# Kernel tuning notes

Hardware: AMD Instinct MI355X
Metric: run time of the kernel (lower is better)

The kernel has to match this reference:

```python
import jax, jax.numpy as jnp
import numpy as np

B, T, D, K = 4, 4096, 256, 16


def hankel_eigvecs(T: int, k: int) -> jnp.ndarray:
    """Top-k |eigenvalue| eigenvectors of Z_ij = 2/((i+j)^3 - (i+j)), 1-indexed."""
    idx = np.arange(1, T + 1, dtype=np.float64)
    ij = idx[None, :] + idx[:, None]
    Z = 2.0 / (ij ** 3 - ij)
    w, v = np.linalg.eigh(Z)
    top = np.argsort(-np.abs(w))[:k]
    return jnp.asarray(v[:, top], dtype=jnp.float32)  # (T, K)


def setup_inputs() -> dict:
    key = jax.random.key(0)
    kx, kw = jax.random.split(key)
    x = jax.random.normal(kx, (B, T, D), dtype=jnp.float32)
    # Stacked weights of the K independent nn.Linear(D, D, bias=False) modules.
    # W[k] is the torch Linear weight (out, in); y = c @ W[k].T.
    W = jax.random.normal(kw, (K, D, D), dtype=jnp.float32) * (1.0 / np.sqrt(D))
    phi = hankel_eigvecs(T, K)  # Hankel eigenvector buffer (non-trainable)
    return {"x": x, "W": W, "phi": phi}


def reference(x, W, phi):
    # x: (B,T,D), W: (K,D,D), phi: (T,K)
    # c_k[t] = cumsum_{s<=t} phi[s,k] * x[s]   -> batched over all K filters
    C = jnp.cumsum(phi[None, :, :, None] * x[:, :, None, :], axis=1)  # (B,T,K,D)
    # out[t] = sum_k phi[t,k] * (c_k[t] @ W_k^T)
    out = jnp.einsum('btkd,ked,tk->bte', C, W, phi)  # (B,T,D)
    return out  # dropout is identity in eval mode (dropout=0.0)
```

## Files before the change

kernel.cpp:

```cpp
#include <hip/hip_runtime.h>


typedef __bf16 bf16x8 __attribute__((ext_vector_type(8)));
typedef float  f32x4  __attribute__((ext_vector_type(4)));
typedef unsigned short u16;
typedef unsigned int   u32;

__device__ static inline u16 f2bf(float f) {
    unsigned int u = __float_as_uint(f);
    u = (u + 0x7fffu + ((u >> 16) & 1u)) >> 16;
    return (u16)u;
}

__device__ static inline void gload16(const void* g, void* l) {
    __builtin_amdgcn_global_load_lds((const __attribute__((address_space(1))) void*)g,
                                     (__attribute__((address_space(3))) void*)l, 16, 0, 0);
}

__global__ __launch_bounds__(256) void k0_wt(const float* __restrict__ W, u16* __restrict__ WT) {
    const int e = blockIdx.x, d = threadIdx.x;
    union { u16 u[16]; uint4 v[2]; } ob;
#pragma unroll
    for (int k = 0; k < 16; ++k)
        ob.u[k] = f2bf(W[((size_t)k * 256 + e) * 256 + d]);
    uint4* dst = (uint4*)(WT + (size_t)e * 4096 + d * 16);
    dst[0] = ob.v[0]; dst[1] = ob.v[1];
}

__global__ __launch_bounds__(256) void k1_sums(const float* __restrict__ x,
                                               const float* __restrict__ phi,
                                               float* __restrict__ U) {
    __shared__ float phis[256];
    const int tid = threadIdx.x;
    const int b = blockIdx.x, c = blockIdx.y;
    const int t0 = c * 16;
    phis[tid] = phi[t0 * 16 + tid];
    __syncthreads();
    float acc[16];
#pragma unroll
    for (int k = 0; k < 16; ++k) acc[k] = 0.f;
    for (int s = 0; s < 16; ++s) {
        const float xv = x[(size_t)((b << 12) + t0 + s) * 256 + tid];
        union { float f[16]; float4 v[4]; } pv;
#pragma unroll
        for (int j = 0; j < 4; ++j) pv.v[j] = *(const float4*)&phis[s * 16 + j * 4];
#pragma unroll
        for (int k = 0; k < 16; ++k) acc[k] = fmaf(pv.f[k], xv, acc[k]);
    }
    float4* Up = (float4*)(U + ((size_t)((b * 256 + c) * 256 + tid)) * 16);
    union { float f[16]; float4 v[4]; } ov;
#pragma unroll
    for (int k = 0; k < 16; ++k) ov.f[k] = acc[k];
#pragma unroll
    for (int j = 0; j < 4; ++j) Up[j] = ov.v[j];
}

__global__ __launch_bounds__(256) void k2_scan(float* __restrict__ U) {
    const int b  = blockIdx.x;
    const int dl = threadIdx.x & 63;
    const int dk = blockIdx.y * 64 + dl;
    const int q  = threadIdx.x >> 6;
    float* base = U + (size_t)b * 1048576 + (size_t)(q * 64) * 4096 + dk;
    float s = 0.f;
#pragma unroll 8
    for (int j = 0; j < 64; ++j) s += base[(size_t)j * 4096];
    __shared__ float qs[4][64];
    qs[q][dl] = s;
    __syncthreads();
    float pre = 0.f;
#pragma unroll
    for (int i = 0; i < 4; ++i) pre += (i < q) ? qs[i][dl] : 0.f;
    float run = pre;
#pragma unroll 8
    for (int j = 0; j < 64; ++j) {
        const float v = base[(size_t)j * 4096];
        base[(size_t)j * 4096] = run;
        run += v;
    }
}

__global__ __launch_bounds__(512, 2) void k4_fused(const float* __restrict__ x,
                                                   const float* __restrict__ phi,
                                                   const float* __restrict__ U,
                                                   const u16* __restrict__ BT,
                                                   float* __restrict__ C) {
    __shared__ __align__(16) char smem[131072];
    const int tid = threadIdx.x;
    const int m0 = blockIdx.x * 128;
    const int ks = blockIdx.y;
    const int b  = m0 >> 12, t0 = m0 & 4095, c0 = t0 >> 4;
    const int w = tid >> 6, l = tid & 63;
    const int wm = (w >> 2) * 64, wn = (w & 3) * 64;
    const int lg = l >> 4, lr = l & 15;
    f32x4 acc[4][4] = {};

    const bool is_chain = (w < 4);
    const bool is_stage = (w >= 4);

    const int kp = l & 7, dl = (l >> 3) & 3, ch = (w << 1) | (l >> 5);
    const int colb = dl * 32 + kp * 4;
    float2 p01[16];
    if (is_chain) {
#pragma unroll
        for (int s = 0; s < 16; ++s)
            p01[s] = *(const float2*)&phi[(t0 + ch * 16 + s) * 16 + kp * 2];
    }

    const int tl = tid & 255;
    const char* bsrc = (const char*)BT + (size_t)(tl >> 3) * 8192 + ks * 4096
                     + (((tl & 7) * 16) ^ (((tl >> 3) & 7) << 4));
    char* const smemA = smem + 98304;

    auto stageB = [&](int kt, int bufw) {
        char* dst = smem + bufw * 32768 + tl * 16;
        const char* src = bsrc + (size_t)kt * 128;
#pragma unroll
        for (int c = 0; c < 8; ++c)
            gload16(src + (size_t)c * 262144, dst + c * 4096);
    };
    auto issueX = [&](float (&xr)[16], float2& us, int kt) {
        const int d = ks * 128 + kt * 4 + dl;
        const float* xp = x + (size_t)(m0 + ch * 16) * 256 + d;
#pragma unroll
        for (int s = 0; s < 16; ++s) xr[s] = xp[(size_t)s * 256];
        us = *(const float2*)&U[((size_t)((b * 256 + c0 + ch) * 256 + d)) * 16 + kp * 2];
    };
    auto chains = [&](const float (&xr)[16], float2 us, int abw) {
        float r0 = us.x, r1 = us.y;
        char* Ab = smemA + abw * 16384 + ch * 2048;
#pragma unroll
        for (int s = 0; s < 16; ++s) {
            r0 = fmaf(p01[s].x, xr[s], r0);
            r1 = fmaf(p01[s].y, xr[s], r1);
            const float v0 = p01[s].x * r0, v1 = p01[s].y * r1;
            u32 pk;
            asm("v_cvt_pk_bf16_f32 %0, %1, %2" : "=v"(pk) : "v"(v0), "v"(v1));
            *(u32*)(Ab + s * 128 + (colb ^ ((s & 7) << 4))) = pk;
        }
    };
    auto mfma_phase = [&](int abr, int bbr) {
        const char* Abase = smemA + abr * 16384;
        const char* Bbase = smem + bbr * 32768;
#pragma unroll
        for (int kk = 0; kk < 2; ++kk) {
            const int kb = kk * 64 + lg * 16;
            bf16x8 af[4], bfv[4];
#pragma unroll
            for (int mi = 0; mi < 4; ++mi) {
                const int r = wm + mi * 16 + lr;
                af[mi] = *(const bf16x8*)(Abase + r * 128 + (kb ^ ((r & 7) << 4)));
            }
#pragma unroll
            for (int ni = 0; ni < 4; ++ni) {
                const int n = wn + ni * 16 + lr;
                bfv[ni] = *(const bf16x8*)(Bbase + n * 128 + (kb ^ ((n & 7) << 4)));
            }
#pragma unroll
            for (int mi = 0; mi < 4; ++mi)
#pragma unroll
                for (int ni = 0; ni < 4; ++ni)
                    acc[mi][ni] = __builtin_amdgcn_mfma_f32_16x16x32_bf16(af[mi], bfv[ni], acc[mi][ni], 0, 0, 0);
        }
    };

    float xA[16], xB[16]; float2 uA, uB;
    if (is_chain) { issueX(xA, uA, 0); issueX(xB, uB, 1); }
    if (is_stage) { stageB(0, 0); stageB(1, 1); }
    __builtin_amdgcn_sched_barrier(0);
    if (is_chain) {
        chains(xA, uA, 0);
        asm volatile("s_waitcnt lgkmcnt(0)" ::: "memory");
    }
    if (is_stage) asm volatile("s_waitcnt vmcnt(8)" ::: "memory");
    asm volatile("s_barrier" ::: "memory");

    int br = 0, bw = 2;
    auto body = [&](int kt, float (&xW)[16], float2& uW,
                    const float (&xR)[16], float2 uR) {
        const int abr = kt & 1;
        if (kt + 2 < 32) {
            if (is_stage)      stageB(kt + 2, bw);
            else if (is_chain) issueX(xW, uW, kt + 2);
        }
        __builtin_amdgcn_sched_barrier(0);
        if (is_chain && (kt + 1 < 32)) chains(xR, uR, abr ^ 1);
        __builtin_amdgcn_s_setprio(1);
        mfma_phase(abr, br);
        __builtin_amdgcn_s_setprio(0);
        if (is_chain) asm volatile("s_waitcnt lgkmcnt(0)" ::: "memory");
        if (is_stage) {
            if (kt + 2 < 32) asm volatile("s_waitcnt vmcnt(8)" ::: "memory");
            else             asm volatile("s_waitcnt vmcnt(0)" ::: "memory");
        }
        if (kt < 31) asm volatile("s_barrier" ::: "memory");
        br = (br == 2) ? 0 : br + 1;
        bw = (bw == 2) ? 0 : bw + 1;
    };

    for (int kt = 0; kt < 32; kt += 2) {
        body(kt,     xA, uA, xB, uB);
        body(kt + 1, xB, uB, xA, uA);
    }

#pragma unroll
    for (int mi = 0; mi < 4; ++mi)
#pragma unroll
        for (int ni = 0; ni < 4; ++ni)
#pragma unroll
            for (int r = 0; r < 4; ++r) {
                const int row = m0 + wm + mi * 16 + lg * 4 + r;
                const int col = wn + ni * 16 + lr;
                unsafeAtomicAdd(&C[(size_t)row * 256 + col], acc[mi][ni][r]);
            }
}

extern "C" void kernel_launch(void* const* d_in, const int* in_sizes, int n_in,
                              void* d_out, int out_size, void* d_ws, size_t ws_size,
                              hipStream_t stream) {
    const float* x   = (const float*)d_in[0];
    const float* W   = (const float*)d_in[1];
    const float* phi = (const float*)d_in[2];
    float* out = (float*)d_out;

    char* ws = (char*)d_ws;
    u16*   WT = (u16*)ws;
    float* U  = (float*)(ws + (2u << 20));

    k0_wt  <<<256, 256, 0, stream>>>(W, WT);
    k1_sums<<<dim3(4, 256), 256, 0, stream>>>(x, phi, U);
    k2_scan<<<dim3(4, 64), 256, 0, stream>>>(U);
    hipMemsetAsync(d_out, 0, (size_t)out_size * sizeof(float), stream);
    k4_fused<<<dim3(128, 2), 512, 0, stream>>>(x, phi, U, WT, out);
}
```

Before: 102.6 us.

## Split each k-step into four barrier-synchronized phases interleaving LDS reads, staging, chains and MFMA

Restructures the fused kernel's main loop so each k-tile iteration is broken into four sub-phases. In each one, fragment LDS reads, a quarter of the B staging loads, a quarter of the chain computation and 8 MFMAs are interleaved under workgroup-wide barriers, in the style of ping-pong scheduling. The aim is to overlap MFMA execution with chain ALU work and memory traffic at finer grain and to lower register pressure from holding all A and B fragments at once. It adds four times as many barriers per iteration, which risks extra synchronisation stalls.

```diff
diff --git a/kernel.cpp b/kernel.cpp
--- a/kernel.cpp
+++ b/kernel.cpp
@@ -16,6 +16,9 @@
     __builtin_amdgcn_global_load_lds((const __attribute__((address_space(1))) void*)g,
                                      (__attribute__((address_space(3))) void*)l, 16, 0, 0);
 }
+
+#define SBAR()  asm volatile("s_barrier" ::: "memory")
+#define LGKM0() asm volatile("s_waitcnt lgkmcnt(0)" ::: "memory")
 
 __global__ __launch_bounds__(256) void k0_wt(const float* __restrict__ W, u16* __restrict__ WT) {
     const int e = blockIdx.x, d = threadIdx.x;
@@ -111,13 +114,6 @@
                      + (((tl & 7) * 16) ^ (((tl >> 3) & 7) << 4));
     char* const smemA = smem + 98304;
 
-    auto stageB = [&](int kt, int bufw) {
-        char* dst = smem + bufw * 32768 + tl * 16;
-        const char* src = bsrc + (size_t)kt * 128;
-#pragma unroll
-        for (int c = 0; c < 8; ++c)
-            gload16(src + (size_t)c * 262144, dst + c * 4096);
-    };
     auto issueX = [&](float (&xr)[16], float2& us, int kt) {
         const int d = ks * 128 + kt * 4 + dl;
         const float* xp = x + (size_t)(m0 + ch * 16) * 256 + d;
@@ -125,77 +121,128 @@
         for (int s = 0; s < 16; ++s) xr[s] = xp[(size_t)s * 256];
         us = *(const float2*)&U[((size_t)((b * 256 + c0 + ch) * 256 + d)) * 16 + kp * 2];
     };
-    auto chains = [&](const float (&xr)[16], float2 us, int abw) {
-        float r0 = us.x, r1 = us.y;
-        char* Ab = smemA + abw * 16384 + ch * 2048;
+
+    bf16x8 bfv[4], af0, af1;
+    auto rdB = [&](const char* Bbase, int kk) {
+        const int kb = kk * 64 + lg * 16;
+#pragma unroll
+        for (int ni = 0; ni < 4; ++ni) {
+            const int n = wn + ni * 16 + lr;
+            bfv[ni] = *(const bf16x8*)(Bbase + n * 128 + (kb ^ ((n & 7) << 4)));
+        }
+    };
+    auto rdA = [&](const char* Abase, int kk, int mh) {
+        const int kb = kk * 64 + lg * 16;
+        const int ra = wm + mh * 32 + lr, rb = ra + 16;
+        af0 = *(const bf16x8*)(Abase + ra * 128 + (kb ^ ((ra & 7) << 4)));
+        af1 = *(const bf16x8*)(Abase + rb * 128 + (kb ^ ((rb & 7) << 4)));
+    };
+    auto mm8 = [&](int mh) {
+        __builtin_amdgcn_s_setprio(1);
+#pragma unroll
+        for (int ni = 0; ni < 4; ++ni)
+            acc[mh * 2][ni] = __builtin_amdgcn_mfma_f32_16x16x32_bf16(af0, bfv[ni], acc[mh * 2][ni], 0, 0, 0);
+#pragma unroll
+        for (int ni = 0; ni < 4; ++ni)
+            acc[mh * 2 + 1][ni] = __builtin_amdgcn_mfma_f32_16x16x32_bf16(af1, bfv[ni], acc[mh * 2 + 1][ni], 0, 0, 0);
+        __builtin_amdgcn_s_setprio(0);
+    };
+
+    int br = 0, bw = 2;
+
+    auto body = [&](int kt, float (&xW)[16], float2& uW,
+                    const float (&xR)[16], float2 uR) {
+        const int abr = kt & 1;
+        const char* Abase = smemA + abr * 16384;
+        const char* Bbase = smem + br * 32768;
+        char* Ab = smemA + (abr ^ 1) * 16384 + ch * 2048;
+        const bool doCh = is_chain && (kt + 1 < 32);
+        const bool doIs = (kt + 2 < 32);
+        float r0 = 0.f, r1 = 0.f;
+        if (doCh) { r0 = uR.x; r1 = uR.y; }
+
+        auto slice = [&](int q) {
+#pragma unroll
+            for (int j = 0; j < 4; ++j) {
+                const int s = q * 4 + j;
+                r0 = fmaf(p01[s].x, xR[s], r0);
+                r1 = fmaf(p01[s].y, xR[s], r1);
+                const float v0 = p01[s].x * r0, v1 = p01[s].y * r1;
+                u32 pk;
+                asm("v_cvt_pk_bf16_f32 %0, %1, %2" : "=v"(pk) : "v"(v0), "v"(v1));
+                *(u32*)(Ab + s * 128 + (colb ^ ((s & 7) << 4))) = pk;
+            }
+        };
+        auto sg = [&](int q) {
+            char* dst = smem + bw * 32768 + tl * 16;
+            const char* src = bsrc + (size_t)(kt + 2) * 128;
+            gload16(src + (size_t)(2 * q) * 262144,     dst + (2 * q) * 4096);
+            gload16(src + (size_t)(2 * q + 1) * 262144, dst + (2 * q + 1) * 4096);
+        };
+
+        rdB(Bbase, 0); rdA(Abase, 0, 0);
+        if (is_stage && doIs) sg(0);
+        if (doCh) slice(0);
+        SBAR(); LGKM0();
+        mm8(0);
+        SBAR();
+        rdA(Abase, 0, 1);
+        if (is_stage && doIs) sg(1);
+        if (is_chain && doIs) issueX(xW, uW, kt + 2);
+        if (doCh) slice(1);
+        SBAR(); LGKM0();
+        mm8(1);
+        SBAR();
+        rdB(Bbase, 1); rdA(Abase, 1, 0);
+        if (is_stage && doIs) sg(2);
+        if (doCh) slice(2);
+        SBAR(); LGKM0();
+        mm8(0);
+        SBAR();
+        rdA(Abase, 1, 1);
+        if (is_stage && doIs) sg(3);
+        if (doCh) slice(3);
+        if (is_chain) LGKM0();
+        SBAR(); LGKM0();
+        mm8(1);
+        if (is_stage) {
+            if (doIs) asm volatile("s_waitcnt vmcnt(8)" ::: "memory");
+            else      asm volatile("s_waitcnt vmcnt(0)" ::: "memory");
+        }
+        if (kt < 31) SBAR();
+        br = (br == 2) ? 0 : br + 1;
+        bw = (bw == 2) ? 0 : bw + 1;
+    };
+
+    float xA[16], xB[16]; float2 uA, uB;
+    if (is_chain) { issueX(xA, uA, 0); issueX(xB, uB, 1); }
+    if (is_stage) {
+#pragma unroll
+        for (int c = 0; c < 8; ++c) {
+            gload16(bsrc + (size_t)c * 262144,        smem + tl * 16 + c * 4096);
+        }
+#pragma unroll
+        for (int c = 0; c < 8; ++c) {
+            gload16(bsrc + 128 + (size_t)c * 262144,  smem + 32768 + tl * 16 + c * 4096);
+        }
+    }
+    __builtin_amdgcn_sched_barrier(0);
+    if (is_chain) {
+        float r0 = uA.x, r1 = uA.y;
+        char* Ab0 = smemA + ch * 2048;
 #pragma unroll
         for (int s = 0; s < 16; ++s) {
-            r0 = fmaf(p01[s].x, xr[s], r0);
-            r1 = fmaf(p01[s].y, xr[s], r1);
+            r0 = fmaf(p01[s].x, xA[s], r0);
+            r1 = fmaf(p01[s].y, xA[s], r1);
             const float v0 = p01[s].x * r0, v1 = p01[s].y * r1;
             u32 pk;
             asm("v_cvt_pk_bf16_f32 %0, %1, %2" : "=v"(pk) : "v"(v0), "v"(v1));
-            *(u32*)(Ab + s * 128 + (colb ^ ((s & 7) << 4))) = pk;
-        }
-    };
-    auto mfma_phase = [&](int abr, int bbr) {
-        const char* Abase = smemA + abr * 16384;
-        const char* Bbase = smem + bbr * 32768;
-#pragma unroll
-        for (int kk = 0; kk < 2; ++kk) {
-            const int kb = kk * 64 + lg * 16;
-            bf16x8 af[4], bfv[4];
-#pragma unroll
-            for (int mi = 0; mi < 4; ++mi) {
-                const int r = wm + mi * 16 + lr;
-                af[mi] = *(const bf16x8*)(Abase + r * 128 + (kb ^ ((r & 7) << 4)));
-            }
-#pragma unroll
-            for (int ni = 0; ni < 4; ++ni) {
-                const int n = wn + ni * 16 + lr;
-                bfv[ni] = *(const bf16x8*)(Bbase + n * 128 + (kb ^ ((n & 7) << 4)));
-            }
-#pragma unroll
-            for (int mi = 0; mi < 4; ++mi)
-#pragma unroll
-                for (int ni = 0; ni < 4; ++ni)
-                    acc[mi][ni] = __builtin_amdgcn_mfma_f32_16x16x32_bf16(af[mi], bfv[ni], acc[mi][ni], 0, 0, 0);
-        }
-    };
-
-    float xA[16], xB[16]; float2 uA, uB;
-    if (is_chain) { issueX(xA, uA, 0); issueX(xB, uB, 1); }
-    if (is_stage) { stageB(0, 0); stageB(1, 1); }
-    __builtin_amdgcn_sched_barrier(0);
-    if (is_chain) {
-        chains(xA, uA, 0);
-        asm volatile("s_waitcnt lgkmcnt(0)" ::: "memory");
+            *(u32*)(Ab0 + s * 128 + (colb ^ ((s & 7) << 4))) = pk;
+        }
+        LGKM0();
     }
     if (is_stage) asm volatile("s_waitcnt vmcnt(8)" ::: "memory");
-    asm volatile("s_barrier" ::: "memory");
-
-    int br = 0, bw = 2;
-    auto body = [&](int kt, float (&xW)[16], float2& uW,
-                    const float (&xR)[16], float2 uR) {
-        const int abr = kt & 1;
-        if (kt + 2 < 32) {
-            if (is_stage)      stageB(kt + 2, bw);
-            else if (is_chain) issueX(xW, uW, kt + 2);
-        }
-        __builtin_amdgcn_sched_barrier(0);
-        if (is_chain && (kt + 1 < 32)) chains(xR, uR, abr ^ 1);
-        __builtin_amdgcn_s_setprio(1);
-        mfma_phase(abr, br);
-        __builtin_amdgcn_s_setprio(0);
-        if (is_chain) asm volatile("s_waitcnt lgkmcnt(0)" ::: "memory");
-        if (is_stage) {
-            if (kt + 2 < 32) asm volatile("s_waitcnt vmcnt(8)" ::: "memory");
-            else             asm volatile("s_waitcnt vmcnt(0)" ::: "memory");
-        }
-        if (kt < 31) asm volatile("s_barrier" ::: "memory");
-        br = (br == 2) ? 0 : br + 1;
-        bw = (bw == 2) ? 0 : bw + 1;
-    };
+    SBAR();
 
     for (int kt = 0; kt < 32; kt += 2) {
         body(kt,     xA, uA, xB, uB);
```

Result: slower. 113.6 us (+10.7%).
